# Optimization experiments

Hardware: AMD Instinct MI355X
Metric: run time of the kernel (lower is better)

Reference implementation:

```python
import jax, jax.numpy as jnp
import numpy as np

B, T_IN, TOKEN_DIM = 8192, 32, 32
EMB, HEADS, DEPTH = 64, 4, 2
PHASE_REP, PHASE_NUM = 32, 8
PH1, PH2 = 128, 64
ENEMY_NUM = 20


def setup_inputs() -> dict:
    key = jax.random.key(0)
    ks = iter(jax.random.split(key, 64))

    def rnd(shape, s=0.05):
        return jax.random.normal(next(ks), shape, dtype=jnp.float32) * s

    z = lambda *s: jnp.zeros(s, jnp.float32)
    o = lambda *s: jnp.ones(s, jnp.float32)
    # orthonormal phase embedding rows (Gram-Schmidt == QR of transpose)
    qm, _ = np.linalg.qr(np.random.default_rng(0).standard_normal((PHASE_REP, PHASE_NUM)))
    d = {
        "inputs": rnd((B, T_IN, TOKEN_DIM), 1.0),
        "hidden_state": rnd((B, 1, EMB), 1.0),
        "p_h": rnd((B, 1, PHASE_REP), 1.0),
        "emb_W": rnd((TOKEN_DIM, EMB)), "emb_b": z(EMB),
        "Wq": rnd((DEPTH, EMB, EMB * HEADS)),
        "Wk": rnd((DEPTH, EMB, EMB * HEADS)),
        "Wv": rnd((DEPTH, EMB, EMB * HEADS)),
        "Wu": rnd((DEPTH, EMB * HEADS, EMB)), "bu": z(DEPTH, EMB),
        "ln1_g": o(DEPTH, EMB), "ln1_b": z(DEPTH, EMB),
        "ff_W1": rnd((DEPTH, EMB, 4 * EMB)), "ff_b1": z(DEPTH, 4 * EMB),
        "ff_W2": rnd((DEPTH, 4 * EMB, EMB)), "ff_b2": z(DEPTH, EMB),
        "ln2_g": o(DEPTH, EMB), "ln2_b": z(DEPTH, EMB),
        "toprobs_W": rnd((EMB, EMB)), "toprobs_b": z(EMB),
        "cls_W1": rnd((EMB + PHASE_REP, PH1)), "cls_b1": z(PH1),
        "cls_W2": rnd((PH1, PH2)), "cls_b2": z(PH2),
        "cls_W3": rnd((PH2, PHASE_NUM)), "cls_b3": z(PHASE_NUM),
        "qself_W": rnd((EMB + PHASE_REP, 6)), "qself_b": z(6),
        "qint_W": rnd((EMB + PHASE_REP, 1)), "qint_b": z(1),
        "p_e_w": jnp.asarray(qm.T, jnp.float32),
        "task_enemy_num": ENEMY_NUM,
        "task_ally_num": 11,
        "test_mode": 1,
    }
    return d


def _ln(x, g, b):
    mu = jnp.mean(x, -1, keepdims=True)
    var = jnp.mean((x - mu) ** 2, -1, keepdims=True)
    return (x - mu) * jax.lax.rsqrt(var + 1e-5) * g + b


def _forward(inputs, hidden_state, p_h, emb_W, emb_b, Wq, Wk, Wv, Wu, bu,
             ln1_g, ln1_b, ff_W1, ff_b1, ff_W2, ff_b2, ln2_g, ln2_b,
             toprobs_W, toprobs_b, cls_W1, cls_b1, cls_W2, cls_b2, cls_W3,
             cls_b3, qself_W, qself_b, qint_W, qint_b, p_e_w, enemy_num):
    tokens = inputs @ emb_W + emb_b                      # [B, T_IN, EMB]
    x = jnp.concatenate([tokens, hidden_state], axis=1)  # [B, T, EMB]
    b, t, e = x.shape
    scale = e ** -0.25
    for i in range(DEPTH):
        q = (x @ Wq[i]).reshape(b, t, HEADS, e) * scale
        k = (x @ Wk[i]).reshape(b, t, HEADS, e) * scale
        v = (x @ Wv[i]).reshape(b, t, HEADS, e)
        dot = jnp.einsum('bqhe,bkhe->bhqk', q, k)        # [B, H, T, T]
        att = jax.nn.softmax(dot, axis=-1)
        out = jnp.einsum('bhqk,bkhe->bqhe', att, v).reshape(b, t, HEADS * e)
        a = out @ Wu[i] + bu[i]
        x = _ln(a + x, ln1_g[i], ln1_b[i])
        f = jax.nn.relu(x @ ff_W1[i] + ff_b1[i]) @ ff_W2[i] + ff_b2[i]
        x = _ln(f + x, ln2_g[i], ln2_b[i])
    outputs = x @ toprobs_W + toprobs_b                  # [B, T, EMB]
    h = outputs[:, -1:, :]                               # [B, 1, EMB]
    zz = jnp.concatenate([h, p_h], axis=-1)
    zz = jax.nn.relu(zz @ cls_W1 + cls_b1)
    zz = jax.nn.relu(zz @ cls_W2 + cls_b2)
    probs = jax.nn.softmax(zz @ cls_W3 + cls_b3, axis=-1)
    p_rep = jnp.squeeze(probs @ p_e_w, axis=1)           # [B, PHASE_REP]
    q_basic = jnp.concatenate([outputs[:, 0, :], p_rep], -1) @ qself_W + qself_b
    en = outputs[:, 1:1 + enemy_num, :]                  # [B, E, EMB]
    pr = jnp.broadcast_to(p_rep[:, None, :], (b, enemy_num, PHASE_REP))
    q_en = (jnp.concatenate([en, pr], -1) @ qint_W + qint_b)[..., 0]
    q = jnp.concatenate([q_basic, q_en], axis=1)         # [B, 6 + E]
    return q, h, p_rep


def reference(inputs, hidden_state, p_h, emb_W, emb_b, Wq, Wk, Wv, Wu, bu,
              ln1_g, ln1_b, ff_W1, ff_b1, ff_W2, ff_b2, ln2_g, ln2_b,
              toprobs_W, toprobs_b, cls_W1, cls_b1, cls_W2, cls_b2, cls_W3,
              cls_b3, qself_W, qself_b, qint_W, qint_b, p_e_w,
              task_enemy_num, task_ally_num, test_mode):
    q, h, p_rep = _forward(inputs, hidden_state, p_h, emb_W, emb_b, Wq, Wk,
                           Wv, Wu, bu, ln1_g, ln1_b, ff_W1, ff_b1, ff_W2,
                           ff_b2, ln2_g, ln2_b, toprobs_W, toprobs_b, cls_W1,
                           cls_b1, cls_W2, cls_b2, cls_W3, cls_b3, qself_W,
                           qself_b, qint_W, qint_b, p_e_w, int(task_enemy_num))
    return (q, h, p_rep, p_rep)
```

## Files before the change

kernel.cpp:

```cpp
#include <hip/hip_runtime.h>
#include <hip/hip_bf16.h>
#include <stdint.h>


typedef __hip_bfloat16 bf16;
using bf16x8 = __attribute__((ext_vector_type(8))) short;
using f32x4  = __attribute__((ext_vector_type(4))) float;

#define BTOT 8192
#define SCL 0.35355339059327373f

__device__ __forceinline__ short f2bf(float f) {
  uint32_t u = __float_as_uint(f);
  return (short)((u + 0x7FFFu + ((u >> 16) & 1u)) >> 16);
}
__device__ __forceinline__ float bf2f(short s) {
  return __uint_as_float(((uint32_t)(uint16_t)s) << 16);
}
__device__ __forceinline__ f32x4 MM(bf16x8 a, bf16x8 b, f32x4 c) {
  return __builtin_amdgcn_mfma_f32_16x16x32_bf16(a, b, c, 0, 0, 0);
}

#define OFF_X   0
#define OFF_Q   11520
#define OFF_K   23184
#define OFF_VT  34848
#define OFF_V32 45088
#define OFF_P   45344
#define OFF_T1  34848
#define OFF_ZZ1 46368
#define OFF_ZZ2 47392
#define OFF_PB  47904
#define OFF_PR  47968
#define OFF_PHB 53024
#define SMEM_SZ 53280

#define WS_EMB 0
#define WS_WQ  256
#define WS_WK  4352
#define WS_WV  8448
#define WS_WU  12544
#define WS_W1  16640
#define WS_W2  20736
#define WS_TOP 24832
#define WS_BYTES 405504

__device__ __forceinline__ bf16x8 LD8(const uint8_t* sm, int off) {
  return *(const bf16x8*)(sm + off);
}
__device__ __forceinline__ void ST16(uint8_t* sm, int off, short v) {
  *(short*)(sm + off) = v;
}
__device__ __forceinline__ short LD16(const uint8_t* sm, int off) {
  return *(const short*)(sm + off);
}

struct PP {
  const float *emb, *wq, *wk, *wvp, *wu, *w1, *w2, *top;
  short* dst;
};

__global__ __launch_bounds__(256) void prep_frags(PP pp) {
  constexpr int START[15] = {0, 2048, 18432, 34816, 51200, 67584, 83968,
                             100352, 116736, 133120, 149504, 165888, 182272,
                             198656, 202752};
  for (int idx = blockIdx.x * 256 + threadIdx.x; idx < 202752;
       idx += gridDim.x * 256) {
#pragma unroll
    for (int t = 0; t < 14; ++t) {
      if (idx >= START[t] && idx < START[t + 1]) {
        int K, N; const float* s;
        switch (t) {
          case 0:  s = pp.emb;          K = 32;  N = 64;  break;
          case 1:  s = pp.wq;           K = 64;  N = 256; break;
          case 2:  s = pp.wq + 16384;   K = 64;  N = 256; break;
          case 3:  s = pp.wk;           K = 64;  N = 256; break;
          case 4:  s = pp.wk + 16384;   K = 64;  N = 256; break;
          case 5:  s = pp.wvp;          K = 64;  N = 256; break;
          case 6:  s = pp.wvp + 16384;  K = 64;  N = 256; break;
          case 7:  s = pp.wu;           K = 256; N = 64;  break;
          case 8:  s = pp.wu + 16384;   K = 256; N = 64;  break;
          case 9:  s = pp.w1;           K = 64;  N = 256; break;
          case 10: s = pp.w1 + 16384;   K = 64;  N = 256; break;
          case 11: s = pp.w2;           K = 256; N = 64;  break;
          case 12: s = pp.w2 + 16384;   K = 256; N = 64;  break;
          default: s = pp.top;          K = 64;  N = 64;  break;
        }
        int rel = idx - START[t];
        int lane = (rel >> 3) & 63, jj = rel & 7, fi = rel >> 9;
        int KS = K >> 5;
        int nt = fi / KS, ks = fi - nt * KS;
        int k = ks * 32 + ((lane >> 4) << 3) + jj;
        int n = nt * 16 + (lane & 15);
        pp.dst[idx] = f2bf(s[(size_t)k * N + n]);
      }
    }
  }
}

struct MP {
  const float *inputs, *hidden, *p_h;
  const float *emb_b, *bu, *ln1_g, *ln1_b, *ff_b1, *ff_b2, *ln2_g, *ln2_b,
      *toprobs_b;
  const float *cls_W1, *cls_b1, *cls_W2, *cls_b2, *cls_W3, *cls_b3;
  const float *qself_W, *qself_b, *qint_W, *qint_b, *p_e_w;
  const bf16x8* ws;
  float* out;
};

__global__ __launch_bounds__(256, 3) void fused_mfma(MP p) {
  __shared__ __align__(16) uint8_t sm[SMEM_SZ];
  const int tid = threadIdx.x;
  const int lane = tid & 63;
  const int wv = tid >> 6;
  const int g16 = lane >> 4;
  const int l15 = lane & 15;
  const int b0 = blockIdx.x * 2;
  const bf16x8* WS = p.ws;

  if (tid < 64) {
    *(float*)(sm + OFF_PHB + tid * 4) =
        p.p_h[(size_t)(b0 + (tid >> 5)) * 32 + (tid & 31)];
  }
  for (int idx = tid; idx < 2048; idx += 256) {
    int r = idx >> 5, c = idx & 31;
    ST16(sm, OFF_T1 + r * 80 + c * 2, f2bf(p.inputs[(size_t)b0 * 1024 + idx]));
  }
  if (tid < 128) {
    int e = tid >> 6, c = tid & 63;
    ST16(sm, OFF_X + (e * 33 + 32) * 144 + c * 2,
         f2bf(p.hidden[(size_t)(b0 + e) * 64 + c]));
  }
  __syncthreads();

  {
    int arow = wv * 16 + l15;
    bf16x8 a = LD8(sm, OFF_T1 + arow * 80 + g16 * 16);
#pragma unroll
    for (int nt = 0; nt < 4; ++nt) {
      int col = nt * 16 + l15;
      float eb = p.emb_b[col];
      f32x4 acc = {eb, eb, eb, eb};
      acc = MM(a, WS[WS_EMB + nt * 64 + lane], acc);
#pragma unroll
      for (int i = 0; i < 4; ++i) {
        int r = wv * 16 + g16 * 4 + i;
        int grow = (r >> 5) * 33 + (r & 31);
        ST16(sm, OFF_X + grow * 144 + col * 2, f2bf(acc[i]));
      }
    }
  }
  __syncthreads();

  const int ea = wv >> 1, sub = wv & 1;
  const int e33 = ea * 33;

  for (int L = 0; L < 2; ++L) {
    const int wq8 = WS_WQ + L * 2048, wk8 = WS_WK + L * 2048,
              wv8 = WS_WV + L * 2048, wu8 = WS_WU + L * 2048,
              w18 = WS_W1 + L * 2048, w28 = WS_W2 + L * 2048;

    f32x4 wu[2][4];
#pragma unroll
    for (int im = 0; im < 2; ++im)
#pragma unroll
      for (int nt = 0; nt < 4; ++nt) {
        float bv = p.bu[L * 64 + nt * 16 + l15];
        wu[im][nt] = {bv, bv, bv, bv};
      }

    for (int h = 0; h < 4; ++h) {
      for (int wid = wv; wid < 20; wid += 4) {
        int mt = wid >> 2, nt = wid & 3;
        int arow = mt * 16 + l15;
        bf16x8 a0 = LD8(sm, OFF_X + arow * 144 + g16 * 16);
        bf16x8 a1 = LD8(sm, OFF_X + arow * 144 + 64 + g16 * 16);
        int col = nt * 16 + l15;
        int rb = mt * 16 + g16 * 4;
        int f0 = (h * 4 + nt) * 2;
        f32x4 q = {0.f, 0.f, 0.f, 0.f}, k = q, v = q;
        q = MM(a0, WS[wq8 + f0 * 64 + lane], q);
        q = MM(a1, WS[wq8 + (f0 + 1) * 64 + lane], q);
        k = MM(a0, WS[wk8 + f0 * 64 + lane], k);
        k = MM(a1, WS[wk8 + (f0 + 1) * 64 + lane], k);
        v = MM(a0, WS[wv8 + f0 * 64 + lane], v);
        v = MM(a1, WS[wv8 + (f0 + 1) * 64 + lane], v);
#pragma unroll
        for (int i = 0; i < 4; ++i) {
          int r = rb + i;
          if (r < 66) {
            ST16(sm, OFF_Q + r * 144 + col * 2, f2bf(q[i] * SCL));
            ST16(sm, OFF_K + r * 144 + col * 2, f2bf(k[i] * SCL));
            int e = (r >= 33) ? 1 : 0;
            int tok = r - e * 33;
            if (tok == 32)
              ST16(sm, OFF_V32 + (e * 64 + col) * 2, f2bf(v[i]));
            else
              ST16(sm, OFF_VT + (e * 64 + col) * 80 + tok * 2, f2bf(v[i]));
          }
        }
      }
      __syncthreads();

      f32x4 S[2][3];
#pragma unroll
      for (int im = 0; im < 2; ++im) {
        if (!(im == 1 && sub)) {
          int mtl = sub + 2 * im;
          int arow = e33 + mtl * 16 + l15;
          bf16x8 a0 = LD8(sm, OFF_Q + arow * 144 + g16 * 16);
          bf16x8 a1 = LD8(sm, OFF_Q + arow * 144 + 64 + g16 * 16);
#pragma unroll
          for (int nt = 0; nt < 3; ++nt) {
            int brow = e33 + nt * 16 + l15;
            bf16x8 b0 = LD8(sm, OFF_K + brow * 144 + g16 * 16);
            bf16x8 b1 = LD8(sm, OFF_K + brow * 144 + 64 + g16 * 16);
            f32x4 acc = {0.f, 0.f, 0.f, 0.f};
            acc = MM(a0, b0, acc);
            acc = MM(a1, b1, acc);
            S[im][nt] = acc;
          }
        }
      }
      float p32sav[2][4];
#pragma unroll
      for (int im = 0; im < 2; ++im) {
        if (!(im == 1 && sub)) {
          int mtl = sub + 2 * im;
#pragma unroll
          for (int i = 0; i < 4; ++i) {
            float v0 = S[im][0][i], v1 = S[im][1][i];
            float v2 = (l15 == 0) ? S[im][2][i] : -1e30f;
            float m = fmaxf(fmaxf(v0, v1), v2);
            m = fmaxf(m, __shfl_xor(m, 1, 64));
            m = fmaxf(m, __shfl_xor(m, 2, 64));
            m = fmaxf(m, __shfl_xor(m, 4, 64));
            m = fmaxf(m, __shfl_xor(m, 8, 64));
            float p0 = __expf(v0 - m), p1 = __expf(v1 - m),
                  p2 = __expf(v2 - m);
            float s = p0 + p1 + p2;
            s += __shfl_xor(s, 1, 64);
            s += __shfl_xor(s, 2, 64);
            s += __shfl_xor(s, 4, 64);
            s += __shfl_xor(s, 8, 64);
            float inv = 1.0f / s;
            p0 *= inv; p1 *= inv; p2 *= inv;
            int prow = ea * 48 + mtl * 16 + g16 * 4 + i;
            ST16(sm, OFF_P + prow * 80 + l15 * 2, f2bf(p0));
            ST16(sm, OFF_P + prow * 80 + (16 + l15) * 2, f2bf(p1));
            p32sav[im][i] = __shfl(p2, lane & 48, 64);
          }
        }
      }
      asm volatile("s_waitcnt lgkmcnt(0)" ::: "memory");
#pragma unroll
      for (int im = 0; im < 2; ++im) {
        if (!(im == 1 && sub)) {
          int mtl = sub + 2 * im;
          bf16x8 pa = LD8(sm, OFF_P + (ea * 48 + mtl * 16 + l15) * 80 + g16 * 16);
#pragma unroll
          for (int nt = 0; nt < 4; ++nt) {
            int col = nt * 16 + l15;
            float v32v = bf2f(LD16(sm, OFF_V32 + (ea * 64 + col) * 2));
            bf16x8 vb = LD8(sm, OFF_VT + (ea * 64 + col) * 80 + g16 * 16);
            f32x4 acc = {0.f, 0.f, 0.f, 0.f};
            acc = MM(pa, vb, acc);
#pragma unroll
            for (int i = 0; i < 4; ++i) {
              float o = acc[i] + p32sav[im][i] * v32v;
              int lr = mtl * 16 + g16 * 4 + i;
              if (lr < 33)
                ST16(sm, OFF_Q + (e33 + lr) * 144 + col * 2, f2bf(o));
            }
          }
        }
      }
      asm volatile("s_waitcnt lgkmcnt(0)" ::: "memory");
#pragma unroll
      for (int im = 0; im < 2; ++im) {
        if (!(im == 1 && sub)) {
          int mtl = sub + 2 * im;
          int arow = e33 + mtl * 16 + l15;
          bf16x8 a0 = LD8(sm, OFF_Q + arow * 144 + g16 * 16);
          bf16x8 a1 = LD8(sm, OFF_Q + arow * 144 + 64 + g16 * 16);
#pragma unroll
          for (int nt = 0; nt < 4; ++nt) {
            wu[im][nt] = MM(a0, WS[wu8 + (nt * 8 + h * 2) * 64 + lane], wu[im][nt]);
            wu[im][nt] = MM(a1, WS[wu8 + (nt * 8 + h * 2 + 1) * 64 + lane], wu[im][nt]);
          }
        }
      }
      __syncthreads();
    }

#pragma unroll
    for (int im = 0; im < 2; ++im) {
      if (!(im == 1 && sub)) {
        int mtl = sub + 2 * im;
#pragma unroll
        for (int i = 0; i < 4; ++i) {
          int lr = mtl * 16 + g16 * 4 + i;
          int grow = e33 + lr;
          bool ok = (lr < 33);
          float v[4];
#pragma unroll
          for (int nt = 0; nt < 4; ++nt) {
            int col = nt * 16 + l15;
            float xr = ok ? bf2f(LD16(sm, OFF_X + grow * 144 + col * 2)) : 0.f;
            v[nt] = wu[im][nt][i] + xr;
          }
          float s = v[0] + v[1] + v[2] + v[3];
          s += __shfl_xor(s, 1, 64); s += __shfl_xor(s, 2, 64);
          s += __shfl_xor(s, 4, 64); s += __shfl_xor(s, 8, 64);
          float mu = s * 0.015625f;
          float q2 = 0.f;
#pragma unroll
          for (int nt = 0; nt < 4; ++nt) { float d = v[nt] - mu; q2 += d * d; }
          q2 += __shfl_xor(q2, 1, 64); q2 += __shfl_xor(q2, 2, 64);
          q2 += __shfl_xor(q2, 4, 64); q2 += __shfl_xor(q2, 8, 64);
          float inv = rsqrtf(q2 * 0.015625f + 1e-5f);
#pragma unroll
          for (int nt = 0; nt < 4; ++nt) {
            int col = nt * 16 + l15;
            float o = (v[nt] - mu) * inv * p.ln1_g[L * 64 + col] + p.ln1_b[L * 64 + col];
            if (ok) ST16(sm, OFF_X + grow * 144 + col * 2, f2bf(o));
          }
        }
      }
    }
    __syncthreads();

    f32x4 ff[2][4];
#pragma unroll
    for (int im = 0; im < 2; ++im)
#pragma unroll
      for (int nt = 0; nt < 4; ++nt) {
        float bv = p.ff_b2[L * 64 + nt * 16 + l15];
        ff[im][nt] = {bv, bv, bv, bv};
      }
#pragma unroll
    for (int cc = 0; cc < 4; ++cc) {
#pragma unroll
      for (int im = 0; im < 2; ++im) {
        if (!(im == 1 && wv != 0)) {
          int mt = im ? 4 : wv;
          int arow = mt * 16 + l15;
          bf16x8 a0 = LD8(sm, OFF_X + arow * 144 + g16 * 16);
          bf16x8 a1 = LD8(sm, OFF_X + arow * 144 + 64 + g16 * 16);
#pragma unroll
          for (int nt = 0; nt < 4; ++nt) {
            float b1 = p.ff_b1[L * 256 + cc * 64 + nt * 16 + l15];
            f32x4 hh = {b1, b1, b1, b1};
            int f0 = (cc * 4 + nt) * 2;
            hh = MM(a0, WS[w18 + f0 * 64 + lane], hh);
            hh = MM(a1, WS[w18 + (f0 + 1) * 64 + lane], hh);
#pragma unroll
            for (int i = 0; i < 4; ++i)
              ST16(sm, OFF_T1 + (mt * 16 + g16 * 4 + i) * 144 + (nt * 16 + l15) * 2,
                   f2bf(fmaxf(hh[i], 0.f)));
          }
          asm volatile("s_waitcnt lgkmcnt(0)" ::: "memory");
          bf16x8 ta = LD8(sm, OFF_T1 + arow * 144 + g16 * 16);
          bf16x8 tb = LD8(sm, OFF_T1 + arow * 144 + 64 + g16 * 16);
#pragma unroll
          for (int nt = 0; nt < 4; ++nt) {
            ff[im][nt] = MM(ta, WS[w28 + (nt * 8 + cc * 2) * 64 + lane], ff[im][nt]);
            ff[im][nt] = MM(tb, WS[w28 + (nt * 8 + cc * 2 + 1) * 64 + lane], ff[im][nt]);
          }
        }
      }
    }
#pragma unroll
    for (int im = 0; im < 2; ++im) {
      if (!(im == 1 && wv != 0)) {
        int mt = im ? 4 : wv;
#pragma unroll
        for (int i = 0; i < 4; ++i) {
          int grow = mt * 16 + g16 * 4 + i;
          bool ok = grow < 66;
          float v[4];
#pragma unroll
          for (int nt = 0; nt < 4; ++nt) {
            int col = nt * 16 + l15;
            float xr = ok ? bf2f(LD16(sm, OFF_X + grow * 144 + col * 2)) : 0.f;
            v[nt] = ff[im][nt][i] + xr;
          }
          float s = v[0] + v[1] + v[2] + v[3];
          s += __shfl_xor(s, 1, 64); s += __shfl_xor(s, 2, 64);
          s += __shfl_xor(s, 4, 64); s += __shfl_xor(s, 8, 64);
          float mu = s * 0.015625f;
          float q2 = 0.f;
#pragma unroll
          for (int nt = 0; nt < 4; ++nt) { float d = v[nt] - mu; q2 += d * d; }
          q2 += __shfl_xor(q2, 1, 64); q2 += __shfl_xor(q2, 2, 64);
          q2 += __shfl_xor(q2, 4, 64); q2 += __shfl_xor(q2, 8, 64);
          float inv = rsqrtf(q2 * 0.015625f + 1e-5f);
#pragma unroll
          for (int nt = 0; nt < 4; ++nt) {
            int col = nt * 16 + l15;
            float o = (v[nt] - mu) * inv * p.ln2_g[L * 64 + col] + p.ln2_b[L * 64 + col];
            if (ok) ST16(sm, OFF_X + grow * 144 + col * 2, f2bf(o));
          }
        }
      }
    }
    __syncthreads();
  }

#pragma unroll
  for (int im = 0; im < 2; ++im) {
    if (!(im == 1 && wv != 0)) {
      int mt = im ? 4 : wv;
      int arow = mt * 16 + l15;
      bf16x8 a0 = LD8(sm, OFF_X + arow * 144 + g16 * 16);
      bf16x8 a1 = LD8(sm, OFF_X + arow * 144 + 64 + g16 * 16);
#pragma unroll
      for (int nt = 0; nt < 4; ++nt) {
        int col = nt * 16 + l15;
        float tb = p.toprobs_b[col];
        f32x4 acc = {tb, tb, tb, tb};
        acc = MM(a0, WS[WS_TOP + (nt * 2) * 64 + lane], acc);
        acc = MM(a1, WS[WS_TOP + (nt * 2 + 1) * 64 + lane], acc);
#pragma unroll
        for (int i = 0; i < 4; ++i) {
          int r = mt * 16 + g16 * 4 + i;
          ST16(sm, OFF_T1 + r * 144 + col * 2, f2bf(acc[i]));
        }
      }
    }
  }
  __syncthreads();

  {
    const int gg = tid >> 7;
    const int j = tid & 127;
    const size_t be = (size_t)(b0 + gg);
    {
      float s = p.cls_b1[j];
      for (int k2 = 0; k2 < 64; ++k2)
        s += bf2f(LD16(sm, OFF_T1 + (gg * 33 + 32) * 144 + k2 * 2)) *
             p.cls_W1[k2 * 128 + j];
      for (int k2 = 0; k2 < 32; ++k2)
        s += *(float*)(sm + OFF_PHB + (gg * 32 + k2) * 4) *
             p.cls_W1[(64 + k2) * 128 + j];
      *(float*)(sm + OFF_ZZ1 + (gg * 128 + j) * 4) = fmaxf(s, 0.f);
    }
    __syncthreads();
    if (j < 64) {
      float s = p.cls_b2[j];
      for (int k2 = 0; k2 < 128; ++k2)
        s += *(float*)(sm + OFF_ZZ1 + (gg * 128 + k2) * 4) * p.cls_W2[k2 * 64 + j];
      *(float*)(sm + OFF_ZZ2 + (gg * 64 + j) * 4) = fmaxf(s, 0.f);
    }
    __syncthreads();
    if (j < 8) {
      float s = p.cls_b3[j];
      for (int k2 = 0; k2 < 64; ++k2)
        s += *(float*)(sm + OFF_ZZ2 + (gg * 64 + k2) * 4) * p.cls_W3[k2 * 8 + j];
      *(float*)(sm + OFF_PB + (gg * 8 + j) * 4) = s;
    }
    __syncthreads();
    if (j == 0) {
      float* pb = (float*)(sm + OFF_PB) + gg * 8;
      float m = pb[0];
#pragma unroll
      for (int k2 = 1; k2 < 8; ++k2) m = fmaxf(m, pb[k2]);
      float sum = 0.f, e8[8];
#pragma unroll
      for (int k2 = 0; k2 < 8; ++k2) { e8[k2] = __expf(pb[k2] - m); sum += e8[k2]; }
      float inv = 1.f / sum;
#pragma unroll
      for (int k2 = 0; k2 < 8; ++k2) pb[k2] = e8[k2] * inv;
    }
    __syncthreads();
    if (j < 32) {
      float s = 0.f;
#pragma unroll
      for (int k2 = 0; k2 < 8; ++k2)
        s += *(float*)(sm + OFF_PB + (gg * 8 + k2) * 4) * p.p_e_w[k2 * 32 + j];
      *(float*)(sm + OFF_PR + (gg * 32 + j) * 4) = s;
      p.out[(size_t)BTOT * 90 + be * 32 + j] = s;
      p.out[(size_t)BTOT * 122 + be * 32 + j] = s;
    }
    __syncthreads();
    if (j < 6) {
      float s = p.qself_b[j];
      for (int k2 = 0; k2 < 64; ++k2)
        s += bf2f(LD16(sm, OFF_T1 + (gg * 33) * 144 + k2 * 2)) * p.qself_W[k2 * 6 + j];
      for (int k2 = 0; k2 < 32; ++k2)
        s += *(float*)(sm + OFF_PR + (gg * 32 + k2) * 4) * p.qself_W[(64 + k2) * 6 + j];
      p.out[be * 26 + j] = s;
    } else if (j >= 6 && j < 26) {
      int en = j - 6;
      float s = p.qint_b[0];
      for (int k2 = 0; k2 < 64; ++k2)
        s += bf2f(LD16(sm, OFF_T1 + (gg * 33 + 1 + en) * 144 + k2 * 2)) * p.qint_W[k2];
      for (int k2 = 0; k2 < 32; ++k2)
        s += *(float*)(sm + OFF_PR + (gg * 32 + k2) * 4) * p.qint_W[64 + k2];
      p.out[be * 26 + 6 + en] = s;
    } else if (j >= 32 && j < 96) {
      int c = j - 32;
      p.out[(size_t)BTOT * 26 + be * 64 + c] =
          bf2f(LD16(sm, OFF_T1 + (gg * 33 + 32) * 144 + c * 2));
    }
  }
}

#define TIN 32
#define TDIM 32
#define T 33
#define E 64
#define NH 4
#define NDEPTH 2

struct FParams {
  const float *inputs, *hidden, *p_h, *emb_W, *emb_b;
  const float *Wq, *Wk, *Wv, *Wu, *bu, *ln1_g, *ln1_b;
  const float *ff_W1, *ff_b1, *ff_W2, *ff_b2, *ln2_g, *ln2_b;
  const float *toprobs_W, *toprobs_b;
  const float *cls_W1, *cls_b1, *cls_W2, *cls_b2, *cls_W3, *cls_b3;
  const float *qself_W, *qself_b, *qint_W, *qint_b, *p_e_w;
  float* out;
};

__global__ __launch_bounds__(256) void fused_fb(FParams p) {
  const int b = blockIdx.x;
  const int tid = threadIdx.x;
  const int lane = tid & 63;
  const int wvv = tid >> 6;

  __shared__ float xb[T * E], t0[T * E], kT[E * T], vbuf[T * E], ab[T * E],
      scb[T * T];
  __shared__ float zz1[128], zz2[64], pbs[8], prs[32], phb[32];

  for (int idx = tid; idx < TIN * TDIM; idx += 256)
    scb[idx] = p.inputs[(size_t)b * TIN * TDIM + idx];
  if (tid < 32) phb[tid] = p.p_h[(size_t)b * 32 + tid];
  __syncthreads();
  {
    float s[8];
#pragma unroll
    for (int j = 0; j < 8; ++j) s[j] = 0.f;
    for (int k = 0; k < TDIM; ++k) {
      float w = p.emb_W[k * E + lane];
#pragma unroll
      for (int j = 0; j < 8; ++j) s[j] += scb[(wvv + 4 * j) * TDIM + k] * w;
    }
    float eb = p.emb_b[lane];
#pragma unroll
    for (int j = 0; j < 8; ++j) xb[(wvv + 4 * j) * E + lane] = s[j] + eb;
    if (wvv == 0) xb[32 * E + lane] = p.hidden[(size_t)b * E + lane];
  }
  __syncthreads();
  const float scale = SCL;
  for (int i = 0; i < NDEPTH; ++i) {
    {
      float bv = p.bu[i * E + lane];
#pragma unroll
      for (int j = 0; j < 9; ++j) {
        int r = wvv + 4 * j;
        if (j < 8 || wvv == 0) ab[r * E + lane] = bv;
      }
    }
    __syncthreads();
    for (int h = 0; h < NH; ++h) {
      const size_t qko = (size_t)i * E * 256 + h * E;
      {
        float sq[9], sk[9], sv[9];
#pragma unroll
        for (int j = 0; j < 9; ++j) { sq[j] = 0; sk[j] = 0; sv[j] = 0; }
        for (int k = 0; k < E; ++k) {
          float wq = p.Wq[qko + k * 256 + lane];
          float wk = p.Wk[qko + k * 256 + lane];
          float wvl = p.Wv[qko + k * 256 + lane];
#pragma unroll
          for (int j = 0; j < 9; ++j) {
            int r = wvv + 4 * j; if (r > 32) r = 32;
            float xv = xb[r * E + k];
            sq[j] += xv * wq; sk[j] += xv * wk; sv[j] += xv * wvl;
          }
        }
#pragma unroll
        for (int j = 0; j < 9; ++j) {
          int r = wvv + 4 * j;
          if (j < 8 || wvv == 0) {
            t0[r * E + lane] = sq[j] * scale;
            kT[lane * T + r] = sk[j] * scale;
            vbuf[r * E + lane] = sv[j];
          }
        }
      }
      __syncthreads();
      if (lane < T) {
        for (int qi = wvv; qi < T; qi += 4) {
          float s = 0.f;
          for (int e = 0; e < E; ++e) s += t0[qi * E + e] * kT[e * T + lane];
          scb[qi * T + lane] = s;
        }
      }
      __syncthreads();
      if (tid < T) {
        float m = -1e30f;
        for (int k2 = 0; k2 < T; ++k2) m = fmaxf(m, scb[tid * T + k2]);
        float sum = 0.f;
        for (int k2 = 0; k2 < T; ++k2) {
          float ev = __expf(scb[tid * T + k2] - m);
          scb[tid * T + k2] = ev; sum += ev;
        }
        float inv = 1.f / sum;
        for (int k2 = 0; k2 < T; ++k2) scb[tid * T + k2] *= inv;
      }
      __syncthreads();
      {
        float s[9];
#pragma unroll
        for (int j = 0; j < 9; ++j) s[j] = 0.f;
        for (int k2 = 0; k2 < T; ++k2) {
          float vload = vbuf[k2 * E + lane];
#pragma unroll
          for (int j = 0; j < 9; ++j) {
            int r = wvv + 4 * j; if (r > 32) r = 32;
            s[j] += scb[r * T + k2] * vload;
          }
        }
#pragma unroll
        for (int j = 0; j < 9; ++j) {
          int r = wvv + 4 * j;
          if (j < 8 || wvv == 0) t0[r * E + lane] = s[j];
        }
      }
      __syncthreads();
      {
        const size_t wuo = (size_t)i * 256 * 64 + (size_t)h * 64 * 64;
        float s[9];
#pragma unroll
        for (int j = 0; j < 9; ++j) s[j] = 0.f;
        for (int k2 = 0; k2 < E; ++k2) {
          float w = p.Wu[wuo + k2 * 64 + lane];
#pragma unroll
          for (int j = 0; j < 9; ++j) {
            int r = wvv + 4 * j; if (r > 32) r = 32;
            s[j] += t0[r * E + k2] * w;
          }
        }
#pragma unroll
        for (int j = 0; j < 9; ++j) {
          int r = wvv + 4 * j;
          if (j < 8 || wvv == 0) ab[r * E + lane] += s[j];
        }
      }
      __syncthreads();
    }
    {
      float gg = p.ln1_g[i * E + lane], bb = p.ln1_b[i * E + lane];
      for (int r = wvv; r < T; r += 4) {
        float v = ab[r * E + lane] + xb[r * E + lane];
// ... 48 lines not shown
          float w = p.ff_W2[w2o + k * 64 + lane];
#pragma unroll
          for (int j = 0; j < 9; ++j) {
            int r = wvv + 4 * j; if (r > 32) r = 32;
            s[j] += t0[r * E + k] * w;
          }
        }
#pragma unroll
        for (int j = 0; j < 9; ++j) {
          int r = wvv + 4 * j;
          if (j < 8 || wvv == 0) ab[r * E + lane] += s[j];
        }
      }
      __syncthreads();
    }
    {
      float gg = p.ln2_g[i * E + lane], bb = p.ln2_b[i * E + lane];
      for (int r = wvv; r < T; r += 4) {
        float v = ab[r * E + lane] + xb[r * E + lane];
        float s = v;
#pragma unroll
        for (int o = 32; o >= 1; o >>= 1) s += __shfl_xor(s, o, 64);
        float mu = s * (1.f / 64.f);
        float d = v - mu, q2 = d * d;
#pragma unroll
        for (int o = 32; o >= 1; o >>= 1) q2 += __shfl_xor(q2, o, 64);
        xb[r * E + lane] = d * (1.f / sqrtf(q2 * (1.f / 64.f) + 1e-5f)) * gg + bb;
      }
    }
    __syncthreads();
  }
  {
    float tb = p.toprobs_b[lane];
    float s[9];
#pragma unroll
    for (int j = 0; j < 9; ++j) s[j] = tb;
    for (int k = 0; k < E; ++k) {
      float w = p.toprobs_W[k * E + lane];
#pragma unroll
      for (int j = 0; j < 9; ++j) {
        int r = wvv + 4 * j; if (r > 32) r = 32;
        s[j] += xb[r * E + k] * w;
      }
    }
#pragma unroll
    for (int j = 0; j < 9; ++j) {
      int r = wvv + 4 * j;
      if (j < 8 || wvv == 0) t0[r * E + lane] = s[j];
    }
  }
  __syncthreads();
  if (tid < 128) {
    float s = p.cls_b1[tid];
    for (int k = 0; k < E; ++k) s += t0[32 * E + k] * p.cls_W1[k * 128 + tid];
    for (int k = 0; k < 32; ++k) s += phb[k] * p.cls_W1[(E + k) * 128 + tid];
    zz1[tid] = fmaxf(s, 0.f);
  }
  __syncthreads();
  if (tid < 64) {
    float s = p.cls_b2[tid];
    for (int k = 0; k < 128; ++k) s += zz1[k] * p.cls_W2[k * 64 + tid];
    zz2[tid] = fmaxf(s, 0.f);
  }
  __syncthreads();
  if (tid < 8) {
    float s = p.cls_b3[tid];
    for (int k = 0; k < 64; ++k) s += zz2[k] * p.cls_W3[k * 8 + tid];
    pbs[tid] = s;
  }
  __syncthreads();
  if (tid == 0) {
    float m = pbs[0];
#pragma unroll
    for (int k = 1; k < 8; ++k) m = fmaxf(m, pbs[k]);
    float e8[8], sum = 0.f;
#pragma unroll
    for (int k = 0; k < 8; ++k) { e8[k] = __expf(pbs[k] - m); sum += e8[k]; }
    float inv = 1.f / sum;
#pragma unroll
    for (int k = 0; k < 8; ++k) pbs[k] = e8[k] * inv;
  }
  __syncthreads();
  if (tid < 32) {
    float s = 0.f;
#pragma unroll
    for (int k = 0; k < 8; ++k) s += pbs[k] * p.p_e_w[k * 32 + tid];
    prs[tid] = s;
    p.out[(size_t)BTOT * 90 + (size_t)b * 32 + tid] = s;
    p.out[(size_t)BTOT * 122 + (size_t)b * 32 + tid] = s;
  }
  __syncthreads();
  if (tid < 6) {
    float s = p.qself_b[tid];
    for (int k = 0; k < E; ++k) s += t0[k] * p.qself_W[k * 6 + tid];
    for (int k = 0; k < 32; ++k) s += prs[k] * p.qself_W[(E + k) * 6 + tid];
    p.out[(size_t)b * 26 + tid] = s;
  }
  if (tid >= 64 && tid < 84) {
    int en = tid - 64;
    float s = p.qint_b[0];
    for (int k = 0; k < E; ++k) s += t0[(1 + en) * E + k] * p.qint_W[k];
    for (int k = 0; k < 32; ++k) s += prs[k] * p.qint_W[E + k];
    p.out[(size_t)b * 26 + 6 + en] = s;
  }
  if (tid >= 128 && tid < 192) {
    int c2 = tid - 128;
    p.out[(size_t)BTOT * 26 + (size_t)b * 64 + c2] = t0[32 * E + c2];
  }
}

extern "C" void kernel_launch(void* const* d_in, const int* in_sizes, int n_in,
                              void* d_out, int out_size, void* d_ws,
                              size_t ws_size, hipStream_t stream) {
  (void)in_sizes; (void)n_in; (void)out_size;
  if (ws_size >= (size_t)WS_BYTES) {
    PP pp;
    pp.emb = (const float*)d_in[3];
    pp.wq = (const float*)d_in[5];
    pp.wk = (const float*)d_in[6];
    pp.wvp = (const float*)d_in[7];
    pp.wu = (const float*)d_in[8];
    pp.w1 = (const float*)d_in[12];
    pp.w2 = (const float*)d_in[14];
    pp.top = (const float*)d_in[18];
    pp.dst = (short*)d_ws;
    hipLaunchKernelGGL(prep_frags, dim3(128), dim3(256), 0, stream, pp);

    MP p;
    p.inputs = (const float*)d_in[0];
    p.hidden = (const float*)d_in[1];
    p.p_h = (const float*)d_in[2];
    p.emb_b = (const float*)d_in[4];
    p.bu = (const float*)d_in[9];
    p.ln1_g = (const float*)d_in[10];
    p.ln1_b = (const float*)d_in[11];
    p.ff_b1 = (const float*)d_in[13];
    p.ff_b2 = (const float*)d_in[15];
    p.ln2_g = (const float*)d_in[16];
    p.ln2_b = (const float*)d_in[17];
    p.toprobs_b = (const float*)d_in[19];
    p.cls_W1 = (const float*)d_in[20];
    p.cls_b1 = (const float*)d_in[21];
    p.cls_W2 = (const float*)d_in[22];
    p.cls_b2 = (const float*)d_in[23];
    p.cls_W3 = (const float*)d_in[24];
    p.cls_b3 = (const float*)d_in[25];
    p.qself_W = (const float*)d_in[26];
    p.qself_b = (const float*)d_in[27];
    p.qint_W = (const float*)d_in[28];
    p.qint_b = (const float*)d_in[29];
    p.p_e_w = (const float*)d_in[30];
    p.ws = (const bf16x8*)d_ws;
    p.out = (float*)d_out;
    hipLaunchKernelGGL(fused_mfma, dim3(BTOT / 2), dim3(256), 0, stream, p);
  } else {
    FParams p;
    p.inputs = (const float*)d_in[0];
    p.hidden = (const float*)d_in[1];
    p.p_h = (const float*)d_in[2];
    p.emb_W = (const float*)d_in[3];
    p.emb_b = (const float*)d_in[4];
    p.Wq = (const float*)d_in[5];
    p.Wk = (const float*)d_in[6];
    p.Wv = (const float*)d_in[7];
    p.Wu = (const float*)d_in[8];
    p.bu = (const float*)d_in[9];
    p.ln1_g = (const float*)d_in[10];
    p.ln1_b = (const float*)d_in[11];
    p.ff_W1 = (const float*)d_in[12];
    p.ff_b1 = (const float*)d_in[13];
    p.ff_W2 = (const float*)d_in[14];
    p.ff_b2 = (const float*)d_in[15];
    p.ln2_g = (const float*)d_in[16];
    p.ln2_b = (const float*)d_in[17];
    p.toprobs_W = (const float*)d_in[18];
    p.toprobs_b = (const float*)d_in[19];
    p.cls_W1 = (const float*)d_in[20];
    p.cls_b1 = (const float*)d_in[21];
    p.cls_W2 = (const float*)d_in[22];
    p.cls_b2 = (const float*)d_in[23];
    p.cls_W3 = (const float*)d_in[24];
    p.cls_b3 = (const float*)d_in[25];
    p.qself_W = (const float*)d_in[26];
    p.qself_b = (const float*)d_in[27];
    p.qint_W = (const float*)d_in[28];
    p.qint_b = (const float*)d_in[29];
    p.p_e_w = (const float*)d_in[30];
    p.out = (float*)d_out;
    hipLaunchKernelGGL(fused_fb, dim3(BTOT), dim3(256), 0, stream, p);
  }
}
```

Before: 575.8 us.

## Double block to 512 threads and redistribute tiles across eight waves

Launches the fused transformer kernel with 8 wavefronts per block instead of 4, reassigning the embedding, QKV, attention, feed-forward and output tiles so each wave handles at most one M-tile, and dropping the per-wave two-tile loops. The aim is shorter per-wave critical paths and more latency hiding within each block. In exchange, several waves sit idle in attention (6 of 8 active) and the feed-forward stage (5 of 8 active). The larger block and the new launch bound of 6 constrain registers per thread and may reduce the number of resident blocks per CU.

```diff
diff --git a/kernel.cpp b/kernel.cpp
--- a/kernel.cpp
+++ b/kernel.cpp
@@ -108,7 +108,7 @@
   float* out;
 };
 
-__global__ __launch_bounds__(256, 3) void fused_mfma(MP p) {
+__global__ __launch_bounds__(512, 6) void fused_mfma(MP p) {
   __shared__ __align__(16) uint8_t sm[SMEM_SZ];
   const int tid = threadIdx.x;
   const int lane = tid & 63;
@@ -122,7 +122,7 @@
     *(float*)(sm + OFF_PHB + tid * 4) =
         p.p_h[(size_t)(b0 + (tid >> 5)) * 32 + (tid & 31)];
   }
-  for (int idx = tid; idx < 2048; idx += 256) {
+  for (int idx = tid; idx < 2048; idx += 512) {
     int r = idx >> 5, c = idx & 31;
     ST16(sm, OFF_T1 + r * 80 + c * 2, f2bf(p.inputs[(size_t)b0 * 1024 + idx]));
   }
@@ -134,17 +134,19 @@
   __syncthreads();
 
   {
-    int arow = wv * 16 + l15;
-    bf16x8 a = LD8(sm, OFF_T1 + arow * 80 + g16 * 16);
-#pragma unroll
-    for (int nt = 0; nt < 4; ++nt) {
+#pragma unroll
+    for (int uu = 0; uu < 2; ++uu) {
+      int u = wv * 2 + uu;
+      int mt = u >> 2, nt = u & 3;
+      int arow = mt * 16 + l15;
+      bf16x8 a = LD8(sm, OFF_T1 + arow * 80 + g16 * 16);
       int col = nt * 16 + l15;
       float eb = p.emb_b[col];
       f32x4 acc = {eb, eb, eb, eb};
       acc = MM(a, WS[WS_EMB + nt * 64 + lane], acc);
 #pragma unroll
       for (int i = 0; i < 4; ++i) {
-        int r = wv * 16 + g16 * 4 + i;
+        int r = mt * 16 + g16 * 4 + i;
         int grow = (r >> 5) * 33 + (r & 31);
         ST16(sm, OFF_X + grow * 144 + col * 2, f2bf(acc[i]));
       }
@@ -152,7 +154,9 @@
   }
   __syncthreads();
 
-  const int ea = wv >> 1, sub = wv & 1;
+  const bool att = wv < 6;
+  const int ea = wv & 1;
+  const int mtl = wv >> 1;
   const int e33 = ea * 33;
 
   for (int L = 0; L < 2; ++L) {
@@ -160,17 +164,15 @@
               wv8 = WS_WV + L * 2048, wu8 = WS_WU + L * 2048,
               w18 = WS_W1 + L * 2048, w28 = WS_W2 + L * 2048;
 
-    f32x4 wu[2][4];
-#pragma unroll
-    for (int im = 0; im < 2; ++im)
-#pragma unroll
-      for (int nt = 0; nt < 4; ++nt) {
-        float bv = p.bu[L * 64 + nt * 16 + l15];
-        wu[im][nt] = {bv, bv, bv, bv};
-      }
+    f32x4 wu[4];
+#pragma unroll
+    for (int nt = 0; nt < 4; ++nt) {
+      float bv = p.bu[L * 64 + nt * 16 + l15];
+      wu[nt] = {bv, bv, bv, bv};
+    }
 
     for (int h = 0; h < 4; ++h) {
-      for (int wid = wv; wid < 20; wid += 4) {
+      for (int wid = wv; wid < 20; wid += 8) {
         int mt = wid >> 2, nt = wid & 3;
         int arow = mt * 16 + l15;
         bf16x8 a0 = LD8(sm, OFF_X + arow * 144 + g16 * 16);
@@ -202,62 +204,50 @@
       }
       __syncthreads();
 
-      f32x4 S[2][3];
-#pragma unroll
-      for (int im = 0; im < 2; ++im) {
-        if (!(im == 1 && sub)) {
-          int mtl = sub + 2 * im;
+      if (att) {
+        f32x4 S[3];
+        {
           int arow = e33 + mtl * 16 + l15;
           bf16x8 a0 = LD8(sm, OFF_Q + arow * 144 + g16 * 16);
           bf16x8 a1 = LD8(sm, OFF_Q + arow * 144 + 64 + g16 * 16);
 #pragma unroll
           for (int nt = 0; nt < 3; ++nt) {
             int brow = e33 + nt * 16 + l15;
-            bf16x8 b0 = LD8(sm, OFF_K + brow * 144 + g16 * 16);
-            bf16x8 b1 = LD8(sm, OFF_K + brow * 144 + 64 + g16 * 16);
+            bf16x8 kb0 = LD8(sm, OFF_K + brow * 144 + g16 * 16);
+            bf16x8 kb1 = LD8(sm, OFF_K + brow * 144 + 64 + g16 * 16);
             f32x4 acc = {0.f, 0.f, 0.f, 0.f};
-            acc = MM(a0, b0, acc);
-            acc = MM(a1, b1, acc);
-            S[im][nt] = acc;
-          }
-        }
-      }
-      float p32sav[2][4];
-#pragma unroll
-      for (int im = 0; im < 2; ++im) {
-        if (!(im == 1 && sub)) {
-          int mtl = sub + 2 * im;
-#pragma unroll
-          for (int i = 0; i < 4; ++i) {
-            float v0 = S[im][0][i], v1 = S[im][1][i];
-            float v2 = (l15 == 0) ? S[im][2][i] : -1e30f;
-            float m = fmaxf(fmaxf(v0, v1), v2);
-            m = fmaxf(m, __shfl_xor(m, 1, 64));
-            m = fmaxf(m, __shfl_xor(m, 2, 64));
-            m = fmaxf(m, __shfl_xor(m, 4, 64));
-            m = fmaxf(m, __shfl_xor(m, 8, 64));
-            float p0 = __expf(v0 - m), p1 = __expf(v1 - m),
-                  p2 = __expf(v2 - m);
-            float s = p0 + p1 + p2;
-            s += __shfl_xor(s, 1, 64);
-            s += __shfl_xor(s, 2, 64);
-            s += __shfl_xor(s, 4, 64);
-            s += __shfl_xor(s, 8, 64);
-            float inv = 1.0f / s;
-            p0 *= inv; p1 *= inv; p2 *= inv;
-            int prow = ea * 48 + mtl * 16 + g16 * 4 + i;
-            ST16(sm, OFF_P + prow * 80 + l15 * 2, f2bf(p0));
-            ST16(sm, OFF_P + prow * 80 + (16 + l15) * 2, f2bf(p1));
-            p32sav[im][i] = __shfl(p2, lane & 48, 64);
-          }
-        }
-      }
-      asm volatile("s_waitcnt lgkmcnt(0)" ::: "memory");
-#pragma unroll
-      for (int im = 0; im < 2; ++im) {
-        if (!(im == 1 && sub)) {
-          int mtl = sub + 2 * im;
-          bf16x8 pa = LD8(sm, OFF_P + (ea * 48 + mtl * 16 + l15) * 80 + g16 * 16);
+            acc = MM(a0, kb0, acc);
+            acc = MM(a1, kb1, acc);
+            S[nt] = acc;
+          }
+        }
+        float p32sav[4];
+#pragma unroll
+        for (int i = 0; i < 4; ++i) {
+          float v0 = S[0][i], v1 = S[1][i];
+          float v2 = (l15 == 0) ? S[2][i] : -1e30f;
+          float m = fmaxf(fmaxf(v0, v1), v2);
+          m = fmaxf(m, __shfl_xor(m, 1, 64));
+          m = fmaxf(m, __shfl_xor(m, 2, 64));
+          m = fmaxf(m, __shfl_xor(m, 4, 64));
+          m = fmaxf(m, __shfl_xor(m, 8, 64));
+          float p0 = __expf(v0 - m), p1 = __expf(v1 - m), p2 = __expf(v2 - m);
+          float s = p0 + p1 + p2;
+          s += __shfl_xor(s, 1, 64);
+          s += __shfl_xor(s, 2, 64);
+          s += __shfl_xor(s, 4, 64);
+          s += __shfl_xor(s, 8, 64);
+          float inv = 1.0f / s;
+          p0 *= inv; p1 *= inv; p2 *= inv;
+          int prow = ea * 48 + mtl * 16 + g16 * 4 + i;
+          ST16(sm, OFF_P + prow * 80 + l15 * 2, f2bf(p0));
+          ST16(sm, OFF_P + prow * 80 + (16 + l15) * 2, f2bf(p1));
+          p32sav[i] = __shfl(p2, lane & 48, 64);
+        }
+        asm volatile("s_waitcnt lgkmcnt(0)" ::: "memory");
+        {
+          bf16x8 pa =
+              LD8(sm, OFF_P + (ea * 48 + mtl * 16 + l15) * 80 + g16 * 16);
 #pragma unroll
           for (int nt = 0; nt < 4; ++nt) {
             int col = nt * 16 + l15;
@@ -267,175 +257,158 @@
             acc = MM(pa, vb, acc);
 #pragma unroll
             for (int i = 0; i < 4; ++i) {
-              float o = acc[i] + p32sav[im][i] * v32v;
+              float o = acc[i] + p32sav[i] * v32v;
               int lr = mtl * 16 + g16 * 4 + i;
               if (lr < 33)
                 ST16(sm, OFF_Q + (e33 + lr) * 144 + col * 2, f2bf(o));
             }
           }
         }
-      }
-      asm volatile("s_waitcnt lgkmcnt(0)" ::: "memory");
-#pragma unroll
-      for (int im = 0; im < 2; ++im) {
-        if (!(im == 1 && sub)) {
-          int mtl = sub + 2 * im;
+        asm volatile("s_waitcnt lgkmcnt(0)" ::: "memory");
+        {
           int arow = e33 + mtl * 16 + l15;
           bf16x8 a0 = LD8(sm, OFF_Q + arow * 144 + g16 * 16);
           bf16x8 a1 = LD8(sm, OFF_Q + arow * 144 + 64 + g16 * 16);
 #pragma unroll
           for (int nt = 0; nt < 4; ++nt) {
-            wu[im][nt] = MM(a0, WS[wu8 + (nt * 8 + h * 2) * 64 + lane], wu[im][nt]);
-            wu[im][nt] = MM(a1, WS[wu8 + (nt * 8 + h * 2 + 1) * 64 + lane], wu[im][nt]);
+            wu[nt] = MM(a0, WS[wu8 + (nt * 8 + h * 2) * 64 + lane], wu[nt]);
+            wu[nt] =
+                MM(a1, WS[wu8 + (nt * 8 + h * 2 + 1) * 64 + lane], wu[nt]);
           }
         }
       }
       __syncthreads();
     }
 
-#pragma unroll
-    for (int im = 0; im < 2; ++im) {
-      if (!(im == 1 && sub)) {
-        int mtl = sub + 2 * im;
-#pragma unroll
-        for (int i = 0; i < 4; ++i) {
-          int lr = mtl * 16 + g16 * 4 + i;
-          int grow = e33 + lr;
-          bool ok = (lr < 33);
-          float v[4];
-#pragma unroll
-          for (int nt = 0; nt < 4; ++nt) {
-            int col = nt * 16 + l15;
-            float xr = ok ? bf2f(LD16(sm, OFF_X + grow * 144 + col * 2)) : 0.f;
-            v[nt] = wu[im][nt][i] + xr;
-          }
-          float s = v[0] + v[1] + v[2] + v[3];
-          s += __shfl_xor(s, 1, 64); s += __shfl_xor(s, 2, 64);
-          s += __shfl_xor(s, 4, 64); s += __shfl_xor(s, 8, 64);
-          float mu = s * 0.015625f;
-          float q2 = 0.f;
-#pragma unroll
-          for (int nt = 0; nt < 4; ++nt) { float d = v[nt] - mu; q2 += d * d; }
-          q2 += __shfl_xor(q2, 1, 64); q2 += __shfl_xor(q2, 2, 64);
-          q2 += __shfl_xor(q2, 4, 64); q2 += __shfl_xor(q2, 8, 64);
-          float inv = rsqrtf(q2 * 0.015625f + 1e-5f);
-#pragma unroll
-          for (int nt = 0; nt < 4; ++nt) {
-            int col = nt * 16 + l15;
-            float o = (v[nt] - mu) * inv * p.ln1_g[L * 64 + col] + p.ln1_b[L * 64 + col];
-            if (ok) ST16(sm, OFF_X + grow * 144 + col * 2, f2bf(o));
-          }
-        }
-      }
-    }
-    __syncthreads();
-
-    f32x4 ff[2][4];
-#pragma unroll
-    for (int im = 0; im < 2; ++im)
-#pragma unroll
-      for (int nt = 0; nt < 4; ++nt) {
-        float bv = p.ff_b2[L * 64 + nt * 16 + l15];
-        ff[im][nt] = {bv, bv, bv, bv};
-      }
+    if (att) {
+#pragma unroll
+      for (int i = 0; i < 4; ++i) {
+        int lr = mtl * 16 + g16 * 4 + i;
+        int grow = e33 + lr;
+        bool ok = (lr < 33);
+        float v[4];
+#pragma unroll
+        for (int nt = 0; nt < 4; ++nt) {
+          int col = nt * 16 + l15;
+          float xr = ok ? bf2f(LD16(sm, OFF_X + grow * 144 + col * 2)) : 0.f;
+          v[nt] = wu[nt][i] + xr;
+        }
+        float s = v[0] + v[1] + v[2] + v[3];
+        s += __shfl_xor(s, 1, 64); s += __shfl_xor(s, 2, 64);
+        s += __shfl_xor(s, 4, 64); s += __shfl_xor(s, 8, 64);
+        float mu = s * 0.015625f;
+        float q2 = 0.f;
+#pragma unroll
+        for (int nt = 0; nt < 4; ++nt) { float d = v[nt] - mu; q2 += d * d; }
+        q2 += __shfl_xor(q2, 1, 64); q2 += __shfl_xor(q2, 2, 64);
+        q2 += __shfl_xor(q2, 4, 64); q2 += __shfl_xor(q2, 8, 64);
+        float inv = rsqrtf(q2 * 0.015625f + 1e-5f);
+#pragma unroll
+        for (int nt = 0; nt < 4; ++nt) {
+          int col = nt * 16 + l15;
+          float o = (v[nt] - mu) * inv * p.ln1_g[L * 64 + col] +
+                    p.ln1_b[L * 64 + col];
+          if (ok) ST16(sm, OFF_X + grow * 144 + col * 2, f2bf(o));
+        }
+      }
+    }
+    __syncthreads();
+
+    f32x4 ff[4];
+#pragma unroll
+    for (int nt = 0; nt < 4; ++nt) {
+      float bv = p.ff_b2[L * 64 + nt * 16 + l15];
+      ff[nt] = {bv, bv, bv, bv};
+    }
+    const bool ffw = wv < 5;
+    const int fmt = wv;
 #pragma unroll
     for (int cc = 0; cc < 4; ++cc) {
-#pragma unroll
-      for (int im = 0; im < 2; ++im) {
-        if (!(im == 1 && wv != 0)) {
-          int mt = im ? 4 : wv;
-          int arow = mt * 16 + l15;
-          bf16x8 a0 = LD8(sm, OFF_X + arow * 144 + g16 * 16);
-          bf16x8 a1 = LD8(sm, OFF_X + arow * 144 + 64 + g16 * 16);
-#pragma unroll
-          for (int nt = 0; nt < 4; ++nt) {
-            float b1 = p.ff_b1[L * 256 + cc * 64 + nt * 16 + l15];
-            f32x4 hh = {b1, b1, b1, b1};
-            int f0 = (cc * 4 + nt) * 2;
-            hh = MM(a0, WS[w18 + f0 * 64 + lane], hh);
-            hh = MM(a1, WS[w18 + (f0 + 1) * 64 + lane], hh);
-#pragma unroll
-            for (int i = 0; i < 4; ++i)
-              ST16(sm, OFF_T1 + (mt * 16 + g16 * 4 + i) * 144 + (nt * 16 + l15) * 2,
-                   f2bf(fmaxf(hh[i], 0.f)));
-          }
-          asm volatile("s_waitcnt lgkmcnt(0)" ::: "memory");
-          bf16x8 ta = LD8(sm, OFF_T1 + arow * 144 + g16 * 16);
-          bf16x8 tb = LD8(sm, OFF_T1 + arow * 144 + 64 + g16 * 16);
-#pragma unroll
-          for (int nt = 0; nt < 4; ++nt) {
-            ff[im][nt] = MM(ta, WS[w28 + (nt * 8 + cc * 2) * 64 + lane], ff[im][nt]);
-            ff[im][nt] = MM(tb, WS[w28 + (nt * 8 + cc * 2 + 1) * 64 + lane], ff[im][nt]);
-          }
-        }
-      }
-    }
-#pragma unroll
-    for (int im = 0; im < 2; ++im) {
-      if (!(im == 1 && wv != 0)) {
-        int mt = im ? 4 : wv;
-#pragma unroll
-        for (int i = 0; i < 4; ++i) {
-          int grow = mt * 16 + g16 * 4 + i;
-          bool ok = grow < 66;
-          float v[4];
-#pragma unroll
-          for (int nt = 0; nt < 4; ++nt) {
-            int col = nt * 16 + l15;
-            float xr = ok ? bf2f(LD16(sm, OFF_X + grow * 144 + col * 2)) : 0.f;
-            v[nt] = ff[im][nt][i] + xr;
-          }
-          float s = v[0] + v[1] + v[2] + v[3];
-          s += __shfl_xor(s, 1, 64); s += __shfl_xor(s, 2, 64);
-          s += __shfl_xor(s, 4, 64); s += __shfl_xor(s, 8, 64);
-          float mu = s * 0.015625f;
-          float q2 = 0.f;
-#pragma unroll
-          for (int nt = 0; nt < 4; ++nt) { float d = v[nt] - mu; q2 += d * d; }
-          q2 += __shfl_xor(q2, 1, 64); q2 += __shfl_xor(q2, 2, 64);
-          q2 += __shfl_xor(q2, 4, 64); q2 += __shfl_xor(q2, 8, 64);
-          float inv = rsqrtf(q2 * 0.015625f + 1e-5f);
-#pragma unroll
-          for (int nt = 0; nt < 4; ++nt) {
-            int col = nt * 16 + l15;
-            float o = (v[nt] - mu) * inv * p.ln2_g[L * 64 + col] + p.ln2_b[L * 64 + col];
-            if (ok) ST16(sm, OFF_X + grow * 144 + col * 2, f2bf(o));
-          }
-        }
-      }
-    }
-    __syncthreads();
-  }
-
-#pragma unroll
-  for (int im = 0; im < 2; ++im) {
-    if (!(im == 1 && wv != 0)) {
-      int mt = im ? 4 : wv;
-      int arow = mt * 16 + l15;
-      bf16x8 a0 = LD8(sm, OFF_X + arow * 144 + g16 * 16);
-      bf16x8 a1 = LD8(sm, OFF_X + arow * 144 + 64 + g16 * 16);
-#pragma unroll
-      for (int nt = 0; nt < 4; ++nt) {
-        int col = nt * 16 + l15;
-        float tb = p.toprobs_b[col];
-        f32x4 acc = {tb, tb, tb, tb};
-        acc = MM(a0, WS[WS_TOP + (nt * 2) * 64 + lane], acc);
-        acc = MM(a1, WS[WS_TOP + (nt * 2 + 1) * 64 + lane], acc);
-#pragma unroll
-        for (int i = 0; i < 4; ++i) {
-          int r = mt * 16 + g16 * 4 + i;
-          ST16(sm, OFF_T1 + r * 144 + col * 2, f2bf(acc[i]));
-        }
-      }
+      if (ffw) {
+        int arow = fmt * 16 + l15;
+        bf16x8 a0 = LD8(sm, OFF_X + arow * 144 + g16 * 16);
+        bf16x8 a1 = LD8(sm, OFF_X + arow * 144 + 64 + g16 * 16);
+#pragma unroll
+        for (int nt = 0; nt < 4; ++nt) {
+          float b1 = p.ff_b1[L * 256 + cc * 64 + nt * 16 + l15];
+          f32x4 hh = {b1, b1, b1, b1};
+          int f0 = (cc * 4 + nt) * 2;
+          hh = MM(a0, WS[w18 + f0 * 64 + lane], hh);
+          hh = MM(a1, WS[w18 + (f0 + 1) * 64 + lane], hh);
+#pragma unroll
+          for (int i = 0; i < 4; ++i)
+            ST16(sm,
+                 OFF_T1 + (fmt * 16 + g16 * 4 + i) * 144 + (nt * 16 + l15) * 2,
+                 f2bf(fmaxf(hh[i], 0.f)));
+        }
+        asm volatile("s_waitcnt lgkmcnt(0)" ::: "memory");
+        bf16x8 ta = LD8(sm, OFF_T1 + arow * 144 + g16 * 16);
+        bf16x8 tb = LD8(sm, OFF_T1 + arow * 144 + 64 + g16 * 16);
+#pragma unroll
+        for (int nt = 0; nt < 4; ++nt) {
+          ff[nt] = MM(ta, WS[w28 + (nt * 8 + cc * 2) * 64 + lane], ff[nt]);
+          ff[nt] = MM(tb, WS[w28 + (nt * 8 + cc * 2 + 1) * 64 + lane], ff[nt]);
+        }
+      }
+    }
+    if (ffw) {
+#pragma unroll
+      for (int i = 0; i < 4; ++i) {
+        int grow = fmt * 16 + g16 * 4 + i;
+        bool ok = grow < 66;
+        float v[4];
+#pragma unroll
+        for (int nt = 0; nt < 4; ++nt) {
+          int col = nt * 16 + l15;
+          float xr = ok ? bf2f(LD16(sm, OFF_X + grow * 144 + col * 2)) : 0.f;
+          v[nt] = ff[nt][i] + xr;
+        }
+        float s = v[0] + v[1] + v[2] + v[3];
+        s += __shfl_xor(s, 1, 64); s += __shfl_xor(s, 2, 64);
+        s += __shfl_xor(s, 4, 64); s += __shfl_xor(s, 8, 64);
+        float mu = s * 0.015625f;
+        float q2 = 0.f;
+#pragma unroll
+        for (int nt = 0; nt < 4; ++nt) { float d = v[nt] - mu; q2 += d * d; }
+        q2 += __shfl_xor(q2, 1, 64); q2 += __shfl_xor(q2, 2, 64);
+        q2 += __shfl_xor(q2, 4, 64); q2 += __shfl_xor(q2, 8, 64);
+        float inv = rsqrtf(q2 * 0.015625f + 1e-5f);
+#pragma unroll
+        for (int nt = 0; nt < 4; ++nt) {
+          int col = nt * 16 + l15;
+          float o = (v[nt] - mu) * inv * p.ln2_g[L * 64 + col] +
+                    p.ln2_b[L * 64 + col];
+          if (ok) ST16(sm, OFF_X + grow * 144 + col * 2, f2bf(o));
+        }
+      }
+    }
+    __syncthreads();
+  }
+
+  for (int wid = wv; wid < 20; wid += 8) {
+    int mt = wid >> 2, nt = wid & 3;
+    int arow = mt * 16 + l15;
+    bf16x8 a0 = LD8(sm, OFF_X + arow * 144 + g16 * 16);
+    bf16x8 a1 = LD8(sm, OFF_X + arow * 144 + 64 + g16 * 16);
+    int col = nt * 16 + l15;
+    float tb = p.toprobs_b[col];
+    f32x4 acc = {tb, tb, tb, tb};
+    acc = MM(a0, WS[WS_TOP + (nt * 2) * 64 + lane], acc);
+    acc = MM(a1, WS[WS_TOP + (nt * 2 + 1) * 64 + lane], acc);
+#pragma unroll
+    for (int i = 0; i < 4; ++i) {
+      int r = mt * 16 + g16 * 4 + i;
+      ST16(sm, OFF_T1 + r * 144 + col * 2, f2bf(acc[i]));
     }
   }
   __syncthreads();
 
   {
-    const int gg = tid >> 7;
+    const bool act = tid < 256;
+    const int gg = (tid >> 7) & 1;
     const int j = tid & 127;
     const size_t be = (size_t)(b0 + gg);
-    {
+    if (act) {
       float s = p.cls_b1[j];
       for (int k2 = 0; k2 < 64; ++k2)
         s += bf2f(LD16(sm, OFF_T1 + (gg * 33 + 32) * 144 + k2 * 2)) *
@@ -446,34 +419,38 @@
       *(float*)(sm + OFF_ZZ1 + (gg * 128 + j) * 4) = fmaxf(s, 0.f);
     }
     __syncthreads();
-    if (j < 64) {
+    if (act && j < 64) {
       float s = p.cls_b2[j];
       for (int k2 = 0; k2 < 128; ++k2)
-        s += *(float*)(sm + OFF_ZZ1 + (gg * 128 + k2) * 4) * p.cls_W2[k2 * 64 + j];
+        s += *(float*)(sm + OFF_ZZ1 + (gg * 128 + k2) * 4) *
+             p.cls_W2[k2 * 64 + j];
       *(float*)(sm + OFF_ZZ2 + (gg * 64 + j) * 4) = fmaxf(s, 0.f);
     }
     __syncthreads();
-    if (j < 8) {
+    if (act && j < 8) {
       float s = p.cls_b3[j];
       for (int k2 = 0; k2 < 64; ++k2)
         s += *(float*)(sm + OFF_ZZ2 + (gg * 64 + k2) * 4) * p.cls_W3[k2 * 8 + j];
       *(float*)(sm + OFF_PB + (gg * 8 + j) * 4) = s;
     }
     __syncthreads();
-    if (j == 0) {
+    if (act && j == 0) {
       float* pb = (float*)(sm + OFF_PB) + gg * 8;
       float m = pb[0];
 #pragma unroll
       for (int k2 = 1; k2 < 8; ++k2) m = fmaxf(m, pb[k2]);
       float sum = 0.f, e8[8];
 #pragma unroll
-      for (int k2 = 0; k2 < 8; ++k2) { e8[k2] = __expf(pb[k2] - m); sum += e8[k2]; }
+      for (int k2 = 0; k2 < 8; ++k2) {
+        e8[k2] = __expf(pb[k2] - m);
+        sum += e8[k2];
+      }
       float inv = 1.f / sum;
 #pragma unroll
       for (int k2 = 0; k2 < 8; ++k2) pb[k2] = e8[k2] * inv;
     }
     __syncthreads();
-    if (j < 32) {
+    if (act && j < 32) {
       float s = 0.f;
 #pragma unroll
       for (int k2 = 0; k2 < 8; ++k2)
@@ -483,25 +460,30 @@
       p.out[(size_t)BTOT * 122 + be * 32 + j] = s;
     }
     __syncthreads();
-    if (j < 6) {
-      float s = p.qself_b[j];
-      for (int k2 = 0; k2 < 64; ++k2)
-        s += bf2f(LD16(sm, OFF_T1 + (gg * 33) * 144 + k2 * 2)) * p.qself_W[k2 * 6 + j];
-      for (int k2 = 0; k2 < 32; ++k2)
-        s += *(float*)(sm + OFF_PR + (gg * 32 + k2) * 4) * p.qself_W[(64 + k2) * 6 + j];
-      p.out[be * 26 + j] = s;
-    } else if (j >= 6 && j < 26) {
-      int en = j - 6;
-      float s = p.qint_b[0];
-      for (int k2 = 0; k2 < 64; ++k2)
-        s += bf2f(LD16(sm, OFF_T1 + (gg * 33 + 1 + en) * 144 + k2 * 2)) * p.qint_W[k2];
-      for (int k2 = 0; k2 < 32; ++k2)
-        s += *(float*)(sm + OFF_PR + (gg * 32 + k2) * 4) * p.qint_W[64 + k2];
-      p.out[be * 26 + 6 + en] = s;
-    } else if (j >= 32 && j < 96) {
-      int c = j - 32;
-      p.out[(size_t)BTOT * 26 + be * 64 + c] =
-          bf2f(LD16(sm, OFF_T1 + (gg * 33 + 32) * 144 + c * 2));
+    if (act) {
+      if (j < 6) {
+        float s = p.qself_b[j];
+        for (int k2 = 0; k2 < 64; ++k2)
+          s += bf2f(LD16(sm, OFF_T1 + (gg * 33) * 144 + k2 * 2)) *
+               p.qself_W[k2 * 6 + j];
+        for (int k2 = 0; k2 < 32; ++k2)
+          s += *(float*)(sm + OFF_PR + (gg * 32 + k2) * 4) *
+               p.qself_W[(64 + k2) * 6 + j];
+        p.out[be * 26 + j] = s;
+      } else if (j >= 6 && j < 26) {
+        int en = j - 6;
+        float s = p.qint_b[0];
+        for (int k2 = 0; k2 < 64; ++k2)
+          s += bf2f(LD16(sm, OFF_T1 + (gg * 33 + 1 + en) * 144 + k2 * 2)) *
+               p.qint_W[k2];
+        for (int k2 = 0; k2 < 32; ++k2)
+          s += *(float*)(sm + OFF_PR + (gg * 32 + k2) * 4) * p.qint_W[64 + k2];
+        p.out[be * 26 + 6 + en] = s;
+      } else if (j >= 32 && j < 96) {
+        int c = j - 32;
+        p.out[(size_t)BTOT * 26 + be * 64 + c] =
+            bf2f(LD16(sm, OFF_T1 + (gg * 33 + 32) * 144 + c * 2));
+      }
     }
   }
 }
@@ -856,7 +838,7 @@
     p.p_e_w = (const float*)d_in[30];
     p.ws = (const bf16x8*)d_ws;
     p.out = (float*)d_out;
-    hipLaunchKernelGGL(fused_mfma, dim3(BTOT / 2), dim3(256), 0, stream, p);
+    hipLaunchKernelGGL(fused_mfma, dim3(BTOT / 2), dim3(512), 0, stream, p);
   } else {
     FParams p;
     p.inputs = (const float*)d_in[0];
```

Result: slower. 877.2 us (+52.3%).
